# Optimization experiments

Measured on AMD Instinct MI355X. Metric: run time of the kernel, lower is better.

## Reference

```python
import jax, jax.numpy as jnp
import numpy as np

EPS = 1e-8       # module epsilon for L1 renormalize
LN_EPS = 1e-5    # torch LayerNorm default eps
NUM_ITER = 3
TEMP = 1.0


def _ln(x, g, b):
    m = x.mean(-1, keepdims=True)
    v = ((x - m) ** 2).mean(-1, keepdims=True)
    return (x - m) * jax.lax.rsqrt(v + LN_EPS) * g + b


def _gru(x, h, W_ih, W_hh, b_ih, b_hh):
    # torch GRUCell: r,z,n gate ordering
    gx = x @ W_ih.T + b_ih
    gh = h @ W_hh.T + b_hh
    xr, xz, xn = jnp.split(gx, 3, axis=-1)
    hr, hz, hn = jnp.split(gh, 3, axis=-1)
    r = jax.nn.sigmoid(xr + hr)
    z = jax.nn.sigmoid(xz + hz)
    n = jnp.tanh(xn + r * hn)
    return (1.0 - z) * n + z * h


def setup_inputs() -> dict:
    key = jax.random.key(0)
    ks = jax.random.split(key, 12)
    B, T, C, S, D, H = 32, 4096, 256, 8, 256, 512

    def xav(k, shape):
        fan_out, fan_in = shape
        lim = (6.0 / (fan_in + fan_out)) ** 0.5
        return jax.random.uniform(k, shape, jnp.float32, -lim, lim)

    return dict(
        inputs=jax.random.normal(ks[0], (B, T, C), jnp.float32),
        slots=jax.random.normal(ks[1], (B, S, D), jnp.float32),
        ln_in_g=jnp.ones((C,), jnp.float32), ln_in_b=jnp.zeros((C,), jnp.float32),
        ln_s_g=jnp.ones((D,), jnp.float32), ln_s_b=jnp.zeros((D,), jnp.float32),
        ln_m_g=jnp.ones((D,), jnp.float32), ln_m_b=jnp.zeros((D,), jnp.float32),
        Wq=xav(ks[2], (D, D)), Wk=xav(ks[3], (D, C)), Wv=xav(ks[4], (D, C)),
        W_ih=xav(ks[5], (3 * D, D)), W_hh=xav(ks[6], (3 * D, D)),
        b_ih=jnp.zeros((3 * D,), jnp.float32), b_hh=jnp.zeros((3 * D,), jnp.float32),
        W1=xav(ks[7], (H, D)), b1=jnp.zeros((H,), jnp.float32),
        W2=xav(ks[8], (D, H)), b2=jnp.zeros((D,), jnp.float32),
    )


def reference(inputs, slots, ln_in_g, ln_in_b, ln_s_g, ln_s_b, ln_m_g, ln_m_b,
              Wq, Wk, Wv, W_ih, W_hh, b_ih, b_hh, W1, b1, W2, b2):
    D = slots.shape[-1]
    x = _ln(inputs, ln_in_g, ln_in_b)           # [B,T,C]
    k = x @ Wk.T                                # [B,T,D]
    v = x @ Wv.T                                # [B,T,D]
    scale = D ** (-0.5)
    logits = attn_sw = None
    for _ in range(NUM_ITER):
        slots_prev = slots
        s = _ln(slots, ln_s_g, ln_s_b)
        q = (s @ Wq.T) * scale                  # [B,S,D]
        logits = jnp.einsum('bsd,btd->bst', q, k)
        attn = jax.nn.softmax(logits / TEMP, axis=1)   # softmax over slots
        a = attn + EPS
        attn_sw = a / a.sum(-1, keepdims=True)         # L1 renorm over tokens
        updates = jnp.einsum('bst,btd->bsd', attn_sw, v)
        slots = _gru(updates, slots_prev, W_ih, W_hh, b_ih, b_hh)
        slots = slots + (jax.nn.relu(_ln(slots, ln_m_g, ln_m_b) @ W1.T + b1) @ W2.T + b2)
    return slots, logits, attn_sw
```

## Files before the change

### kernel.cpp

```cpp
#include <hip/hip_runtime.h>
#include <cstdint>
#include <cstddef>

typedef __bf16 bf16;
typedef float  f32x4  __attribute__((ext_vector_type(4)));
typedef __bf16 bf16x8 __attribute__((ext_vector_type(8)));
typedef __bf16 bf16x4 __attribute__((ext_vector_type(4)));

__global__ __launch_bounds__(256) void k_prep1(
    const float* __restrict__ slots_in, const float* __restrict__ W1,
    const float* __restrict__ W2,
    float* __restrict__ slots, bf16* __restrict__ W1T, bf16* __restrict__ W2T)
{
    const int i = blockIdx.x * 256 + threadIdx.x;
    if      (i <  65536) { slots[i] = slots_in[i]; }
    else if (i < 196608) { int j = i -  65536; int k = j >> 9, c = j & 511;
                           W1T[j] = (bf16)W1[c*256 + k]; }
    else if (i < 327680) { int j = i - 196608; int k = j >> 8, c = j & 255;
                           W2T[j] = (bf16)W2[c*512 + k]; }
}

__global__ __launch_bounds__(256) void k_prep2(
    const float* __restrict__ Wq, const float* __restrict__ Wk,
    const float* __restrict__ W_ih, const float* __restrict__ Wv,
    bf16* __restrict__ Mqk, float* __restrict__ Wxg)
{
    const int c = threadIdx.x;
    __shared__ float v[256];
    if (blockIdx.x < 256) {
        const int e = blockIdx.x;
        v[c] = Wq[(size_t)c*256 + e];
        __syncthreads();
        float a = 0.f;
#pragma unroll 8
        for (int d = 0; d < 256; ++d) a += v[d] * Wk[(size_t)d*256 + c];
        Mqk[(size_t)e*256 + c] = (bf16)(a * 0.0625f);
    } else {
        const int g = blockIdx.x - 256;
        v[c] = W_ih[(size_t)g*256 + c];
        __syncthreads();
        float a = 0.f;
#pragma unroll 8
        for (int d = 0; d < 256; ++d) a += v[d] * Wv[(size_t)d*256 + c];
        Wxg[(size_t)g*256 + c] = a;
    }
}

__global__ __launch_bounds__(256) void k_prep3(
    const float* __restrict__ Wxg, const float* __restrict__ W_hh,
    bf16* __restrict__ WgT)
{
    const int j = blockIdx.x * 256 + threadIdx.x;
    const int k = j / 1536, col = j - k*1536;
    WgT[j] = (bf16)((col < 768) ? Wxg[(size_t)col*256 + k] : W_hh[(size_t)(col-768)*256 + k]);
}

__global__ __launch_bounds__(256) void k_ln_in(
    const float* __restrict__ x, const float* __restrict__ g,
    const float* __restrict__ b, bf16* __restrict__ xln)
{
    const int wave = threadIdx.x >> 6, lane = threadIdx.x & 63;
    const size_t row = (size_t)blockIdx.x * 4 + wave;
    const float* xr = x + row * 256 + lane * 4;
    f32x4 v = *(const f32x4*)xr;
    float s  = v[0] + v[1] + v[2] + v[3];
    float ss = v[0]*v[0] + v[1]*v[1] + v[2]*v[2] + v[3]*v[3];
#pragma unroll
    for (int m = 32; m >= 1; m >>= 1) { s += __shfl_xor(s, m); ss += __shfl_xor(ss, m); }
    const float mean = s * (1.f/256.f);
    const float var  = ss * (1.f/256.f) - mean*mean;
    const float rstd = rsqrtf(var + 1e-5f);
    const f32x4 gg = *(const f32x4*)(g + lane*4);
    const f32x4 bb = *(const f32x4*)(b + lane*4);
    bf16x4 o;
#pragma unroll
    for (int e = 0; e < 4; ++e) o[e] = (bf16)((v[e]-mean)*rstd*gg[e] + bb[e]);
    *(bf16x4*)(xln + row*256 + lane*4) = o;
}

__device__ __forceinline__ void gemv8(const bf16* __restrict__ wp, int LDW,
                                      const float* __restrict__ sp, int klen4,
                                      float* __restrict__ ac)
{
#pragma unroll 8
    for (int k4 = 0; k4 < klen4; ++k4) {
        const f32x4 sv = *(const f32x4*)(sp + k4*4);
#pragma unroll
        for (int kk = 0; kk < 4; ++kk) {
            const bf16x8 w = *(const bf16x8*)(wp + (size_t)(k4*4+kk)*LDW);
#pragma unroll
            for (int j = 0; j < 8; ++j) ac[j] += sv[kk]*(float)w[j];
        }
    }
}

__global__ __launch_bounds__(256) void k_q0(
    const float* __restrict__ slots, const bf16* __restrict__ Mqk,
    const float* __restrict__ g_s, const float* __restrict__ b_s,
    bf16* __restrict__ q2bf, float* __restrict__ den)
{
    const int bs = blockIdx.x, tid = threadIdx.x;
    __shared__ float sln[256], part[2048], red[8];
    const float v0 = slots[(size_t)bs*256 + tid];
    if (tid == 0) den[bs] = 0.f;
    {
        float s1 = v0, s2 = v0*v0;
#pragma unroll
        for (int m = 32; m >= 1; m >>= 1) { s1 += __shfl_xor(s1, m); s2 += __shfl_xor(s2, m); }
        if ((tid & 63) == 0) { red[tid >> 6] = s1; red[4 + (tid >> 6)] = s2; }
    }
    __syncthreads();
    {
        const float mean = (red[0]+red[1]+red[2]+red[3])*(1.f/256.f);
        const float var  = (red[4]+red[5]+red[6]+red[7])*(1.f/256.f) - mean*mean;
        const float rstd = rsqrtf(var + 1e-5f);
        sln[tid] = (v0-mean)*rstd*g_s[tid] + b_s[tid];
    }
    __syncthreads();
    {
        const int g8 = tid & 31, ks = tid >> 5;
        float ac[8] = {0,0,0,0,0,0,0,0};
        gemv8(Mqk + (size_t)(ks*32)*256 + g8*8, 256, sln + ks*32, 8, ac);
#pragma unroll
        for (int j = 0; j < 8; ++j) part[ks*256 + g8*8 + j] = ac[j];
    }
    __syncthreads();
    {
        float a = 0.f;
#pragma unroll
        for (int k = 0; k < 8; ++k) a += part[k*256 + tid];
        q2bf[(size_t)bs*256 + tid] = (bf16)a;
    }
}

__global__ __launch_bounds__(256) void k_attn1(
    const bf16* __restrict__ xln, const bf16* __restrict__ q2bf,
    bf16* __restrict__ abuf, float* __restrict__ den,
    float* __restrict__ logits_out, int write_logits)
{
    const int chunk = blockIdx.x, b = blockIdx.y;
    const int wv = threadIdx.x >> 6, lane = threadIdx.x & 63;
    const int sA = lane & 15;
    const int ko = (lane >> 4) * 8;

    bf16x8 aq[8];
    if (sA < 8) {
#pragma unroll
        for (int kk = 0; kk < 8; ++kk)
            aq[kk] = *(const bf16x8*)(q2bf + (size_t)(b*8 + sA)*256 + kk*32 + ko);
    } else {
#pragma unroll
        for (int kk = 0; kk < 8; ++kk) aq[kk] = (bf16x8){0,0,0,0,0,0,0,0};
    }

    float dacc[4] = {0.f, 0.f, 0.f, 0.f};
#pragma unroll
    for (int it = 0; it < 4; ++it) {
        const int t0 = chunk*256 + wv*64 + it*16;
        f32x4 acc = {0.f, 0.f, 0.f, 0.f};
        const bf16* xp = xln + (size_t)(b*4096 + t0 + sA)*256 + ko;
#pragma unroll
        for (int kk = 0; kk < 8; ++kk) {
            const bf16x8 bfr = *(const bf16x8*)(xp + kk*32);
            acc = __builtin_amdgcn_mfma_f32_16x16x32_bf16(aq[kk], bfr, acc, 0, 0, 0);
        }
        if (lane < 32) {
            float m1 = fmaxf(fmaxf(acc[0], acc[1]), fmaxf(acc[2], acc[3]));
            const float m2 = __shfl_xor(m1, 16);
            const float mx = fmaxf(m1, m2);
            float e[4], s4 = 0.f;
#pragma unroll
            for (int r = 0; r < 4; ++r) { e[r] = expf(acc[r] - mx); s4 += e[r]; }
            const float so = __shfl_xor(s4, 16);
            const float inv = 1.f / (s4 + so);
            const int t = t0 + (lane & 15);
            bf16x4 ab;
#pragma unroll
            for (int r = 0; r < 4; ++r) {
                const float av = e[r]*inv + 1e-8f;
                dacc[r] += av;
                ab[r] = (bf16)av;
            }
            *(bf16x4*)(abuf + (size_t)(b*4096 + t)*8 + (lane >> 4)*4) = ab;
            if (write_logits) {
#pragma unroll
                for (int r = 0; r < 4; ++r)
                    logits_out[(size_t)(b*8 + (lane >> 4)*4 + r)*4096 + t] = acc[r];
            }
        }
    }
    if (lane < 32) {
#pragma unroll
        for (int r = 0; r < 4; ++r) {
            float v = dacc[r];
            v += __shfl_xor(v, 1); v += __shfl_xor(v, 2);
            v += __shfl_xor(v, 4); v += __shfl_xor(v, 8);
            if ((lane & 15) == 0) atomicAdd(&den[b*8 + (lane >> 4)*4 + r], v);
        }
    }
}

__global__ __launch_bounds__(256) void k_attn2(
    const bf16* __restrict__ xln, const bf16* __restrict__ abuf,
    float* __restrict__ numpart)
{
    const int chunk = blockIdx.x, b = blockIdx.y, tid = threadIdx.x;
    __shared__ float alds[8][132];
    if (tid < 128) {
        const bf16x8 a8 = *(const bf16x8*)(abuf + (size_t)(b*4096 + chunk*128 + tid)*8);
#pragma unroll
        for (int s = 0; s < 8; ++s) alds[s][tid] = (float)a8[s];
    }
    __syncthreads();

    const int s2 = tid >> 5, u = tid & 31;
    float nacc[8] = {0,0,0,0,0,0,0,0};
    const bf16* xp = xln + (size_t)(b*4096 + chunk*128)*256 + u*8;
#pragma unroll 8
    for (int t = 0; t < 128; ++t) {
        bf16x8 x8 = *(const bf16x8*)(xp + (size_t)t*256);
        const float a = alds[s2][t];
#pragma unroll
        for (int j = 0; j < 8; ++j) nacc[j] += a * (float)x8[j];
    }
    float* np = numpart + (((size_t)b*32 + chunk)*8 + s2)*256 + u*8;
    *(f32x4*)np       = (f32x4){nacc[0], nacc[1], nacc[2], nacc[3]};
    *(f32x4*)(np + 4) = (f32x4){nacc[4], nacc[5], nacc[6], nacc[7]};
}

__global__ __launch_bounds__(256) void k_attnsw(
    const float* __restrict__ logits, const float* __restrict__ den,
    float* __restrict__ attn_out)
{
    const int chunk = blockIdx.x, b = blockIdx.y;
    const int t = chunk*256 + threadIdx.x;
    float l[8];
#pragma unroll
    for (int s = 0; s < 8; ++s) l[s] = logits[(size_t)(b*8 + s)*4096 + t];
    float mx = l[0];
#pragma unroll
    for (int s = 1; s < 8; ++s) mx = fmaxf(mx, l[s]);
    float e[8], sum = 0.f;
#pragma unroll
    for (int s = 0; s < 8; ++s) { e[s] = expf(l[s] - mx); sum += e[s]; }
    const float inv = 1.f/sum;
#pragma unroll
    for (int s = 0; s < 8; ++s)
        attn_out[(size_t)(b*8 + s)*4096 + t] = (e[s]*inv + 1e-8f) / den[b*8 + s];
}

__global__ __launch_bounds__(512) void k_slot(
    const float* __restrict__ numpart, float* __restrict__ den,
    float* __restrict__ slots,
    const bf16* __restrict__ WgT,
    const float* __restrict__ b_ih, const float* __restrict__ b_hh,
    const float* __restrict__ g_m, const float* __restrict__ b_m,
    const bf16* __restrict__ W1T, const float* __restrict__ b1,
    const bf16* __restrict__ W2T, const float* __restrict__ b2,
    const bf16* __restrict__ Mqk,
    const float* __restrict__ g_s, const float* __restrict__ b_s,
    bf16* __restrict__ q2bf, float* __restrict__ out_slots, int last)
{
    const int bs = blockIdx.x, b = bs >> 3, s = bs & 7;
    const int tid = threadIdx.x;
    __shared__ float HS[256], ynd[256], G[1536], hpr[256];
    __shared__ float hln[256], hid[512], sln[256];
    __shared__ float part[4096];
    __shared__ float red[8];
    __shared__ float dsc;

    {
        const int h = tid >> 8, d2 = tid & 255;
        float a = 0.f;
        const float* np = numpart + (((size_t)b*32 + h*16)*8 + s)*256 + d2;
#pragma unroll 8
        for (int c = 0; c < 16; ++c) a += np[(size_t)c*2048];
        part[h*256 + d2] = a;
        if (tid < 256) HS[tid] = slots[(size_t)bs*256 + tid];
        if (tid == 0) { dsc = den[bs]; den[bs] = 0.f; }
    }
    __syncthreads();
    if (tid < 256) ynd[tid] = (part[tid] + part[256 + tid]) / dsc;
    __syncthreads();

    if (tid < 384) {
        const int g8 = tid % 192, ks = tid / 192;
        const int col = g8*8;
        const float* sp = ((col < 768) ? ynd : HS) + ks*128;
        float ac[8] = {0,0,0,0,0,0,0,0};
        gemv8(WgT + (size_t)(ks*128)*1536 + col, 1536, sp, 32, ac);
#pragma unroll
        for (int j = 0; j < 8; ++j) part[ks*1536 + col + j] = ac[j];
    }
    __syncthreads();
    for (int t = tid; t < 1536; t += 512) {
        const float bias = (t < 768) ? b_ih[t] : b_hh[t - 768];
        G[t] = part[t] + part[1536 + t] + bias;
    }
    __syncthreads();

    if (tid < 256) {
        const float r = 1.f/(1.f + expf(-(G[tid]       + G[768  + tid])));
        const float z = 1.f/(1.f + expf(-(G[256 + tid] + G[1024 + tid])));
        const float n = tanhf(G[512 + tid] + r*G[1280 + tid]);
        hpr[tid] = (1.f - z)*n + z*HS[tid];
    }
    __syncthreads();

    if (tid < 256) {
        const float v = hpr[tid];
        float s1 = v, s2 = v*v;
#pragma unroll
        for (int m = 32; m >= 1; m >>= 1) { s1 += __shfl_xor(s1, m); s2 += __shfl_xor(s2, m); }
        if ((tid & 63) == 0) { red[tid >> 6] = s1; red[4 + (tid >> 6)] = s2; }
    }
    __syncthreads();
    if (tid < 256) {
        const float mean = (red[0]+red[1]+red[2]+red[3])*(1.f/256.f);
        const float var  = (red[4]+red[5]+red[6]+red[7])*(1.f/256.f) - mean*mean;
        const float rstd = rsqrtf(var + 1e-5f);
        hln[tid] = (hpr[tid]-mean)*rstd*g_m[tid] + b_m[tid];
    }
    __syncthreads();

    {
        const int g8 = tid & 63, ks = tid >> 6;
        float ac[8] = {0,0,0,0,0,0,0,0};
        gemv8(W1T + (size_t)(ks*32)*512 + g8*8, 512, hln + ks*32, 8, ac);
#pragma unroll
        for (int j = 0; j < 8; ++j) part[ks*512 + g8*8 + j] = ac[j];
    }
    __syncthreads();
    {
        float a = b1[tid];
#pragma unroll
        for (int k = 0; k < 8; ++k) a += part[k*512 + tid];
        hid[tid] = fmaxf(a, 0.f);
    }
    __syncthreads();

    {
        const int g8 = tid & 31, ks = tid >> 5;
        float ac[8] = {0,0,0,0,0,0,0,0};
        gemv8(W2T + (size_t)(ks*32)*256 + g8*8, 256, hid + ks*32, 8, ac);
#pragma unroll
        for (int j = 0; j < 8; ++j) part[ks*256 + g8*8 + j] = ac[j];
    }
    __syncthreads();
    if (tid < 256) {
        float a = 0.f;
#pragma unroll
        for (int k = 0; k < 16; ++k) a += part[k*256 + tid];
        const float val = hpr[tid] + a + b2[tid];
        HS[tid] = val;
        slots[(size_t)bs*256 + tid] = val;
        if (last) out_slots[(size_t)bs*256 + tid] = val;
    }
    __syncthreads();
    if (last) return;

    if (tid < 256) {
        const float v = HS[tid];
        float s1 = v, s2 = v*v;
#pragma unroll
        for (int m = 32; m >= 1; m >>= 1) { s1 += __shfl_xor(s1, m); s2 += __shfl_xor(s2, m); }
        if ((tid & 63) == 0) { red[tid >> 6] = s1; red[4 + (tid >> 6)] = s2; }
    }
    __syncthreads();
    if (tid < 256) {
        const float mean = (red[0]+red[1]+red[2]+red[3])*(1.f/256.f);
        const float var  = (red[4]+red[5]+red[6]+red[7])*(1.f/256.f) - mean*mean;
        const float rstd = rsqrtf(var + 1e-5f);
        sln[tid] = (HS[tid]-mean)*rstd*g_s[tid] + b_s[tid];
    }
    __syncthreads();

    {
        const int g8 = tid & 31, ks = tid >> 5;
        float ac[8] = {0,0,0,0,0,0,0,0};
        gemv8(Mqk + (size_t)(ks*16)*256 + g8*8, 256, sln + ks*16, 4, ac);
#pragma unroll
        for (int j = 0; j < 8; ++j) part[ks*256 + g8*8 + j] = ac[j];
    }
    __syncthreads();
    if (tid < 256) {
        float a = 0.f;
#pragma unroll
        for (int k = 0; k < 16; ++k) a += part[k*256 + tid];
        q2bf[(size_t)bs*256 + tid] = (bf16)a;
    }
}

extern "C" void kernel_launch(void* const* d_in, const int* in_sizes, int n_in,
                              void* d_out, int out_size, void* d_ws, size_t ws_size,
                              hipStream_t stream)
{
    const float* x        = (const float*)d_in[0];
    const float* slots_in = (const float*)d_in[1];
    const float* ln_in_g  = (const float*)d_in[2];
    const float* ln_in_b  = (const float*)d_in[3];
    const float* ln_s_g   = (const float*)d_in[4];
    const float* ln_s_b   = (const float*)d_in[5];
    const float* ln_m_g   = (const float*)d_in[6];
    const float* ln_m_b   = (const float*)d_in[7];
    const float* Wq       = (const float*)d_in[8];
    const float* Wk       = (const float*)d_in[9];
    const float* Wv       = (const float*)d_in[10];
    const float* W_ih     = (const float*)d_in[11];
    const float* W_hh     = (const float*)d_in[12];
    const float* b_ih     = (const float*)d_in[13];
    const float* b_hh     = (const float*)d_in[14];
    const float* W1       = (const float*)d_in[15];
    const float* b1       = (const float*)d_in[16];
    const float* W2       = (const float*)d_in[17];
    const float* b2       = (const float*)d_in[18];

    float* out_slots  = (float*)d_out;
    float* out_logits = out_slots + 65536;
    float* out_attn   = out_logits + 1048576;

    char* w = (char*)d_ws;
    bf16*  xln     = (bf16*)w;   w += 67108864;
    bf16*  q2bf    = (bf16*)w;   w += 131072;
    bf16*  abuf    = (bf16*)w;   w += 2097152;
    float* slots   = (float*)w;  w += 262144;
    bf16*  WgT     = (bf16*)w;   w += 786432;
    bf16*  W1T     = (bf16*)w;   w += 262144;
    bf16*  W2T     = (bf16*)w;   w += 262144;
    bf16*  Mqk     = (bf16*)w;   w += 131072;
    float* Wxg     = (float*)w;  w += 786432;
    float* numpart = (float*)w;  w += 8388608;
    float* den     = (float*)w;  w += 4096;
    if ((size_t)(w - (char*)d_ws) > ws_size) return;

    k_prep1<<<1280, 256, 0, stream>>>(slots_in, W1, W2, slots, W1T, W2T);
    k_prep2<<<1024, 256, 0, stream>>>(Wq, Wk, W_ih, Wv, Mqk, Wxg);
    k_prep3<<<1536, 256, 0, stream>>>(Wxg, W_hh, WgT);
    k_ln_in<<<32768, 256, 0, stream>>>(x, ln_in_g, ln_in_b, xln);
    k_q0<<<256, 256, 0, stream>>>(slots, Mqk, ln_s_g, ln_s_b, q2bf, den);

    for (int it = 0; it < 3; ++it) {
        const int last = (it == 2);
        k_attn1<<<dim3(16, 32), 256, 0, stream>>>(xln, q2bf, abuf, den, out_logits, last);
        k_attn2<<<dim3(32, 32), 256, 0, stream>>>(xln, abuf, numpart);
        if (last)
            k_attnsw<<<dim3(16, 32), 256, 0, stream>>>(out_logits, den, out_attn);
        k_slot<<<256, 512, 0, stream>>>(numpart, den, slots,
                                        WgT, b_ih, b_hh,
                                        ln_m_g, ln_m_b, W1T, b1, W2T, b2,
                                        Mqk, ln_s_g, ln_s_b,
                                        q2bf, out_slots, last);
    }
}
```

Before: 291.7 us.

## Use MFMA for attention-weighted value accumulation with transposed normalized inputs

Adds a one-time transpose of the layer-normalized inputs into a channel-major buffer. The attention-update kernel is rewritten to use 16x16x32 bf16 MFMA instructions over 512-token chunks, replacing the scalar FMA loop, which cuts partial-sum chunks from 32 to 8 per batch. The aim is to move the per-iteration reduction onto the matrix cores and shrink the partial buffer that the slot kernel reads. In exchange it adds a 64 MB transposed copy plus an extra transpose pass, and half of each MFMA's rows are padding because there are only 8 slots.

```diff
diff --git a/kernel.cpp b/kernel.cpp
--- a/kernel.cpp
+++ b/kernel.cpp
@@ -78,6 +78,36 @@
     *(bf16x4*)(xln + row*256 + lane*4) = o;
 }
 
+__global__ __launch_bounds__(256) void k_tr(
+    const bf16* __restrict__ xln, bf16* __restrict__ xlnT)
+{
+    const int tt = blockIdx.x, ct = blockIdx.y, b = blockIdx.z;
+    const int tid = threadIdx.x;
+    __shared__ __align__(16) char tile[64*128];
+    {
+        const int row = tid >> 2, cq = (tid & 3) * 16;
+        const bf16* src = xln + ((size_t)(b*4096 + tt*64 + row))*256 + ct*64 + cq;
+        bf16x8 v0 = *(const bf16x8*)src;
+        bf16x8 v1 = *(const bf16x8*)(src + 8);
+        const int swz = (row & 7) << 4;
+        *(bf16x8*)(tile + row*128 + ((cq*2)      ^ swz)) = v0;
+        *(bf16x8*)(tile + row*128 + ((cq*2 + 16) ^ swz)) = v1;
+    }
+    __syncthreads();
+    {
+        const int c = tid & 63, tq = tid >> 6;
+        bf16 val[16];
+#pragma unroll
+        for (int j = 0; j < 16; ++j) {
+            const int t = tq*16 + j;
+            val[j] = *(const bf16*)(tile + t*128 + ((2*c) ^ ((t & 7) << 4)));
+        }
+        bf16* dst = xlnT + ((size_t)(b*256 + ct*64 + c))*4096 + tt*64 + tq*16;
+        *(bf16x8*)dst       = *(bf16x8*)&val[0];
+        *(bf16x8*)(dst + 8) = *(bf16x8*)&val[8];
+    }
+}
+
 __device__ __forceinline__ void gemv8(const bf16* __restrict__ wp, int LDW,
                                       const float* __restrict__ sp, int klen4,
                                       float* __restrict__ ac)
@@ -201,31 +231,48 @@
 }
 
 __global__ __launch_bounds__(256) void k_attn2(
-    const bf16* __restrict__ xln, const bf16* __restrict__ abuf,
+    const bf16* __restrict__ xlnT, const bf16* __restrict__ abuf,
     float* __restrict__ numpart)
 {
     const int chunk = blockIdx.x, b = blockIdx.y, tid = threadIdx.x;
-    __shared__ float alds[8][132];
-    if (tid < 128) {
-        const bf16x8 a8 = *(const bf16x8*)(abuf + (size_t)(b*4096 + chunk*128 + tid)*8);
-#pragma unroll
-        for (int s = 0; s < 8; ++s) alds[s][tid] = (float)a8[s];
-    }
-    __syncthreads();
-
-    const int s2 = tid >> 5, u = tid & 31;
-    float nacc[8] = {0,0,0,0,0,0,0,0};
-    const bf16* xp = xln + (size_t)(b*4096 + chunk*128)*256 + u*8;
-#pragma unroll 8
-    for (int t = 0; t < 128; ++t) {
-        bf16x8 x8 = *(const bf16x8*)(xp + (size_t)t*256);
-        const float a = alds[s2][t];
-#pragma unroll
-        for (int j = 0; j < 8; ++j) nacc[j] += a * (float)x8[j];
-    }
-    float* np = numpart + (((size_t)b*32 + chunk)*8 + s2)*256 + u*8;
-    *(f32x4*)np       = (f32x4){nacc[0], nacc[1], nacc[2], nacc[3]};
-    *(f32x4*)(np + 4) = (f32x4){nacc[4], nacc[5], nacc[6], nacc[7]};
+    const int wv = tid >> 6, lane = tid & 63;
+    __shared__ __align__(16) bf16 aT[8][528];
+
+#pragma unroll
+    for (int r = 0; r < 2; ++r) {
+        const int t = r*256 + tid;
+        const bf16x8 a8 = *(const bf16x8*)(abuf + ((size_t)b*4096 + chunk*512 + t)*8);
+#pragma unroll
+        for (int s = 0; s < 8; ++s) aT[s][t] = a8[s];
+    }
+    __syncthreads();
+
+    const int sA = lane & 15, ko = (lane >> 4) * 8;
+    f32x4 acc[4] = {{0,0,0,0},{0,0,0,0},{0,0,0,0},{0,0,0,0}};
+#pragma unroll 4
+    for (int kt = 0; kt < 16; ++kt) {
+        bf16x8 af;
+        if (sA < 8) af = *(const bf16x8*)&aT[sA][kt*32 + ko];
+        else        af = (bf16x8){0,0,0,0,0,0,0,0};
+#pragma unroll
+        for (int i = 0; i < 4; ++i) {
+            const int c = (wv + i*4)*16 + sA;
+            const bf16x8 bfr = *(const bf16x8*)(
+                xlnT + ((size_t)(b*256 + c))*4096 + chunk*512 + kt*32 + ko);
+            acc[i] = __builtin_amdgcn_mfma_f32_16x16x32_bf16(af, bfr, acc[i], 0, 0, 0);
+        }
+    }
+    if (lane < 32) {
+#pragma unroll
+        for (int i = 0; i < 4; ++i) {
+            const int c = (wv + i*4)*16 + (lane & 15);
+#pragma unroll
+            for (int r = 0; r < 4; ++r) {
+                const int s = (lane >> 4)*4 + r;
+                numpart[(((size_t)b*8 + chunk)*8 + s)*256 + c] = acc[i][r];
+            }
+        }
+    }
 }
 
 __global__ __launch_bounds__(256) void k_attnsw(
@@ -272,9 +319,9 @@
     {
         const int h = tid >> 8, d2 = tid & 255;
         float a = 0.f;
-        const float* np = numpart + (((size_t)b*32 + h*16)*8 + s)*256 + d2;
-#pragma unroll 8
-        for (int c = 0; c < 16; ++c) a += np[(size_t)c*2048];
+        const float* np = numpart + (((size_t)b*8 + h*4)*8 + s)*256 + d2;
+#pragma unroll
+        for (int c = 0; c < 4; ++c) a += np[(size_t)c*2048];
         part[h*256 + d2] = a;
         if (tid < 256) HS[tid] = slots[(size_t)bs*256 + tid];
         if (tid == 0) { dsc = den[bs]; den[bs] = 0.f; }
@@ -421,6 +468,7 @@
 
     char* w = (char*)d_ws;
     bf16*  xln     = (bf16*)w;   w += 67108864;
+    bf16*  xlnT    = (bf16*)w;   w += 67108864;
     bf16*  q2bf    = (bf16*)w;   w += 131072;
     bf16*  abuf    = (bf16*)w;   w += 2097152;
     float* slots   = (float*)w;  w += 262144;
@@ -429,7 +477,7 @@
     bf16*  W2T     = (bf16*)w;   w += 262144;
     bf16*  Mqk     = (bf16*)w;   w += 131072;
     float* Wxg     = (float*)w;  w += 786432;
-    float* numpart = (float*)w;  w += 8388608;
+    float* numpart = (float*)w;  w += 2097152;
     float* den     = (float*)w;  w += 4096;
     if ((size_t)(w - (char*)d_ws) > ws_size) return;
 
@@ -437,12 +485,13 @@
     k_prep2<<<1024, 256, 0, stream>>>(Wq, Wk, W_ih, Wv, Mqk, Wxg);
     k_prep3<<<1536, 256, 0, stream>>>(Wxg, W_hh, WgT);
     k_ln_in<<<32768, 256, 0, stream>>>(x, ln_in_g, ln_in_b, xln);
+    k_tr<<<dim3(64, 4, 32), 256, 0, stream>>>(xln, xlnT);
     k_q0<<<256, 256, 0, stream>>>(slots, Mqk, ln_s_g, ln_s_b, q2bf, den);
 
     for (int it = 0; it < 3; ++it) {
         const int last = (it == 2);
         k_attn1<<<dim3(16, 32), 256, 0, stream>>>(xln, q2bf, abuf, den, out_logits, last);
-        k_attn2<<<dim3(32, 32), 256, 0, stream>>>(xln, abuf, numpart);
+        k_attn2<<<dim3(8, 32), 256, 0, stream>>>(xlnT, abuf, numpart);
         if (last)
             k_attnsw<<<dim3(16, 32), 256, 0, stream>>>(out_logits, den, out_attn);
         k_slot<<<256, 512, 0, stream>>>(numpart, den, slots,
```

Result: slower. 305.1 us (+4.6%).

## Fuse attention logits and weighted-sum kernels, staging x tile in LDS

Applied to the files above, without the earlier changes.

Merges k_attn1 and k_attn2 into one kernel. Each block handles 128 tokens, stores the loaded xln tile in swizzled shared memory while computing the logits MFMA, and keeps the attention weights in LDS as fp32. It then computes the weighted numerator from LDS without reading xln a second time from global memory, and drops the bf16 abuf round trip. The cost is 64KB+ of LDS per block, which lowers occupancy, and an extra barrier inside the kernel.

```diff
diff --git a/kernel.cpp b/kernel.cpp
--- a/kernel.cpp
+++ b/kernel.cpp
@@ -133,15 +133,18 @@
     }
 }
 
-__global__ __launch_bounds__(256) void k_attn1(
+__global__ __launch_bounds__(256) void k_attn(
     const bf16* __restrict__ xln, const bf16* __restrict__ q2bf,
-    bf16* __restrict__ abuf, float* __restrict__ den,
+    float* __restrict__ numpart, float* __restrict__ den,
     float* __restrict__ logits_out, int write_logits)
 {
     const int chunk = blockIdx.x, b = blockIdx.y;
-    const int wv = threadIdx.x >> 6, lane = threadIdx.x & 63;
+    const int tid = threadIdx.x;
+    const int wv = tid >> 6, lane = tid & 63;
     const int sA = lane & 15;
     const int ko = (lane >> 4) * 8;
+    __shared__ __align__(16) char  vbuf[128*512];
+    __shared__           float alds[8][132];
 
     bf16x8 aq[8];
     if (sA < 8) {
@@ -155,13 +158,18 @@
 
     float dacc[4] = {0.f, 0.f, 0.f, 0.f};
 #pragma unroll
-    for (int it = 0; it < 4; ++it) {
-        const int t0 = chunk*256 + wv*64 + it*16;
+    for (int it = 0; it < 2; ++it) {
+        const int tl0 = wv*32 + it*16;
+        const int t0  = chunk*128 + tl0;
+        const int tl  = tl0 + sA;
+        char* vrow = vbuf + tl*512;
+        const int swz = (tl & 7) << 4;
         f32x4 acc = {0.f, 0.f, 0.f, 0.f};
         const bf16* xp = xln + (size_t)(b*4096 + t0 + sA)*256 + ko;
 #pragma unroll
         for (int kk = 0; kk < 8; ++kk) {
             const bf16x8 bfr = *(const bf16x8*)(xp + kk*32);
+            *(bf16x8*)(vrow + ((2*(ko + kk*32)) ^ swz)) = bfr;
             acc = __builtin_amdgcn_mfma_f32_16x16x32_bf16(aq[kk], bfr, acc, 0, 0, 0);
         }
         if (lane < 32) {
@@ -173,19 +181,17 @@
             for (int r = 0; r < 4; ++r) { e[r] = expf(acc[r] - mx); s4 += e[r]; }
             const float so = __shfl_xor(s4, 16);
             const float inv = 1.f / (s4 + so);
-            const int t = t0 + (lane & 15);
-            bf16x4 ab;
+            const int tcol = tl0 + (lane & 15);
 #pragma unroll
             for (int r = 0; r < 4; ++r) {
                 const float av = e[r]*inv + 1e-8f;
                 dacc[r] += av;
-                ab[r] = (bf16)av;
+                alds[(lane >> 4)*4 + r][tcol] = av;
             }
-            *(bf16x4*)(abuf + (size_t)(b*4096 + t)*8 + (lane >> 4)*4) = ab;
             if (write_logits) {
 #pragma unroll
                 for (int r = 0; r < 4; ++r)
-                    logits_out[(size_t)(b*8 + (lane >> 4)*4 + r)*4096 + t] = acc[r];
+                    logits_out[(size_t)(b*8 + (lane >> 4)*4 + r)*4096 + chunk*128 + tcol] = acc[r];
             }
         }
     }
@@ -198,34 +204,22 @@
             if ((lane & 15) == 0) atomicAdd(&den[b*8 + (lane >> 4)*4 + r], v);
         }
     }
-}
-
-__global__ __launch_bounds__(256) void k_attn2(
-    const bf16* __restrict__ xln, const bf16* __restrict__ abuf,
-    float* __restrict__ numpart)
-{
-    const int chunk = blockIdx.x, b = blockIdx.y, tid = threadIdx.x;
-    __shared__ float alds[8][132];
-    if (tid < 128) {
-        const bf16x8 a8 = *(const bf16x8*)(abuf + (size_t)(b*4096 + chunk*128 + tid)*8);
-#pragma unroll
-        for (int s = 0; s < 8; ++s) alds[s][tid] = (float)a8[s];
-    }
-    __syncthreads();
-
-    const int s2 = tid >> 5, u = tid & 31;
-    float nacc[8] = {0,0,0,0,0,0,0,0};
-    const bf16* xp = xln + (size_t)(b*4096 + chunk*128)*256 + u*8;
+    __syncthreads();
+
+    {
+        const int s2 = tid >> 5, u = tid & 31;
+        float nacc[8] = {0,0,0,0,0,0,0,0};
 #pragma unroll 8
-    for (int t = 0; t < 128; ++t) {
-        bf16x8 x8 = *(const bf16x8*)(xp + (size_t)t*256);
-        const float a = alds[s2][t];
-#pragma unroll
-        for (int j = 0; j < 8; ++j) nacc[j] += a * (float)x8[j];
-    }
-    float* np = numpart + (((size_t)b*32 + chunk)*8 + s2)*256 + u*8;
-    *(f32x4*)np       = (f32x4){nacc[0], nacc[1], nacc[2], nacc[3]};
-    *(f32x4*)(np + 4) = (f32x4){nacc[4], nacc[5], nacc[6], nacc[7]};
+        for (int t = 0; t < 128; ++t) {
+            const bf16x8 x8 = *(const bf16x8*)(vbuf + t*512 + ((u*16) ^ ((t & 7) << 4)));
+            const float a = alds[s2][t];
+#pragma unroll
+            for (int j = 0; j < 8; ++j) nacc[j] += a * (float)x8[j];
+        }
+        float* np = numpart + (((size_t)b*32 + chunk)*8 + s2)*256 + u*8;
+        *(f32x4*)np       = (f32x4){nacc[0], nacc[1], nacc[2], nacc[3]};
+        *(f32x4*)(np + 4) = (f32x4){nacc[4], nacc[5], nacc[6], nacc[7]};
+    }
 }
 
 __global__ __launch_bounds__(256) void k_attnsw(
@@ -422,7 +416,6 @@
     char* w = (char*)d_ws;
     bf16*  xln     = (bf16*)w;   w += 67108864;
     bf16*  q2bf    = (bf16*)w;   w += 131072;
-    bf16*  abuf    = (bf16*)w;   w += 2097152;
     float* slots   = (float*)w;  w += 262144;
     bf16*  WgT     = (bf16*)w;   w += 786432;
     bf16*  W1T     = (bf16*)w;   w += 262144;
@@ -441,8 +434,7 @@
 
     for (int it = 0; it < 3; ++it) {
         const int last = (it == 2);
-        k_attn1<<<dim3(16, 32), 256, 0, stream>>>(xln, q2bf, abuf, den, out_logits, last);
-        k_attn2<<<dim3(32, 32), 256, 0, stream>>>(xln, abuf, numpart);
+        k_attn<<<dim3(32, 32), 256, 0, stream>>>(xln, q2bf, numpart, den, out_logits, last);
         if (last)
             k_attnsw<<<dim3(16, 32), 256, 0, stream>>>(out_logits, den, out_attn);
         k_slot<<<256, 512, 0, stream>>>(numpart, den, slots,
```

Result: slower. 343.9 us (+17.9%).

## Restructure attn2 so each thread reuses loaded x across all slots

Applied to the files above, without the earlier changes.

The attention-weighted value accumulation kernel previously had each thread handle one slot and eight channels, so each x row was loaded eight times, once per slot group. Each thread now loads four channels of a quarter of the tokens once and accumulates all eight slots. The four token-group partials are then reduced through a 32 KB shared-memory buffer before writing. This cuts redundant global and L2 reads of x. In exchange it uses more registers, adds LDS traffic and an extra barrier, and the larger shared allocation may lower occupancy.

```diff
diff --git a/kernel.cpp b/kernel.cpp
--- a/kernel.cpp
+++ b/kernel.cpp
@@ -206,6 +206,8 @@
 {
     const int chunk = blockIdx.x, b = blockIdx.y, tid = threadIdx.x;
     __shared__ float alds[8][132];
+    __shared__ __align__(16) float part[4][2048];
+
     if (tid < 128) {
         const bf16x8 a8 = *(const bf16x8*)(abuf + (size_t)(b*4096 + chunk*128 + tid)*8);
 #pragma unroll
@@ -213,19 +215,44 @@
     }
     __syncthreads();
 
-    const int s2 = tid >> 5, u = tid & 31;
-    float nacc[8] = {0,0,0,0,0,0,0,0};
-    const bf16* xp = xln + (size_t)(b*4096 + chunk*128)*256 + u*8;
-#pragma unroll 8
-    for (int t = 0; t < 128; ++t) {
-        bf16x8 x8 = *(const bf16x8*)(xp + (size_t)t*256);
-        const float a = alds[s2][t];
-#pragma unroll
-        for (int j = 0; j < 8; ++j) nacc[j] += a * (float)x8[j];
-    }
-    float* np = numpart + (((size_t)b*32 + chunk)*8 + s2)*256 + u*8;
-    *(f32x4*)np       = (f32x4){nacc[0], nacc[1], nacc[2], nacc[3]};
-    *(f32x4*)(np + 4) = (f32x4){nacc[4], nacc[5], nacc[6], nacc[7]};
+    const int tg = tid >> 6, cg = tid & 63;
+    float acc[8][4];
+#pragma unroll
+    for (int s = 0; s < 8; ++s) {
+#pragma unroll
+        for (int j = 0; j < 4; ++j) acc[s][j] = 0.f;
+    }
+
+    const bf16* xp = xln + (size_t)(b*4096 + chunk*128 + tg*32)*256 + cg*4;
+#pragma unroll 4
+    for (int t = 0; t < 32; ++t) {
+        const bf16x4 x4 = *(const bf16x4*)(xp + (size_t)t*256);
+        float xf[4];
+#pragma unroll
+        for (int e = 0; e < 4; ++e) xf[e] = (float)x4[e];
+#pragma unroll
+        for (int s = 0; s < 8; ++s) {
+            const float a = alds[s][tg*32 + t];
+#pragma unroll
+            for (int j = 0; j < 4; ++j) acc[s][j] += a * xf[j];
+        }
+    }
+#pragma unroll
+    for (int s = 0; s < 8; ++s) {
+        const f32x4 v = {acc[s][0], acc[s][1], acc[s][2], acc[s][3]};
+        *(f32x4*)&part[tg][s*256 + cg*4] = v;
+    }
+    __syncthreads();
+
+#pragma unroll
+    for (int o = 0; o < 2; ++o) {
+        const int idx = (tid*2 + o)*4;
+        f32x4 v = *(const f32x4*)&part[0][idx];
+#pragma unroll
+        for (int g = 1; g < 4; ++g) v += *(const f32x4*)&part[g][idx];
+        const int s = idx >> 8, c = idx & 255;
+        *(f32x4*)&numpart[(((size_t)b*32 + chunk)*8 + s)*256 + c] = v;
+    }
 }
 
 __global__ __launch_bounds__(256) void k_attnsw(
```

New measurement: 270.7 us. 7.2% less time.
